# Optimization experiments

Hardware: AMD Instinct MI355X
Metric: run time of the kernel (lower is better)

Reference implementation:

```python
import jax, jax.numpy as jnp
import numpy as np

N, K = 262144, 8
IN_F, H_F, OUT_F = 16, 128, 16
NEG_SLOPE = 0.01  # torch LeakyReLU default


def setup_inputs() -> dict:
    key = jax.random.key(0)
    ks = jax.random.split(key, 10)
    h = jax.random.normal(ks[0], (N, IN_F), dtype=jnp.float32)
    pos = jax.random.uniform(ks[1], (N, 3), dtype=jnp.float32)
    nbr_idx = jax.random.randint(ks[2], (N, K), 0, N)

    def xavier(k, shape):
        fan_in, fan_out = shape[0], shape[1]
        a = jnp.sqrt(6.0 / (fan_in + fan_out))
        return jax.random.uniform(k, shape, jnp.float32, -a, a)

    W0 = xavier(ks[3], (K * IN_F, H_F))
    b0 = xavier(ks[4], (1, H_F))
    W1 = xavier(ks[5], (K * H_F, H_F))
    b1 = xavier(ks[6], (1, H_F))
    W2 = xavier(ks[7], (K * H_F, OUT_F))
    b2 = xavier(ks[8], (1, OUT_F))
    return {"h": h, "pos": pos, "nbr_idx": nbr_idx,
            "W0": W0, "b0": b0, "W1": W1, "b1": b1, "W2": W2, "b2": b2}


def _layer(h, pos, nbr_idx, W, b, activation):
    # gather neighbor messages and positions: [N, K, F], [N, K, 3]
    msgs = h[nbr_idx]
    src_pos = pos[nbr_idx]
    diff = pos[:, None, :] - src_pos                       # [N, K, 3]
    dist = jnp.sqrt(jnp.sum(diff * diff, axis=2, keepdims=True))  # [N, K, 1]
    dist = jnp.where(dist == 0, jnp.float32(0.5), dist)
    wow = (msgs / dist).reshape(h.shape[0], -1)            # [N, K*F]
    out = wow @ W + b
    if activation:
        out = jnp.where(out >= 0, out, NEG_SLOPE * out)
    return out


def reference(h, pos, nbr_idx, W0, b0, W1, b1, W2, b2):
    h1 = _layer(h, pos, nbr_idx, W0, b0, False)   # input layer
    h2 = _layer(h1, pos, nbr_idx, W1, b1, True)   # hidden layer (LeakyReLU)
    h3 = _layer(h2, pos, nbr_idx, W2, b2, False)  # output layer
    return h3
```

## Files before the change

kernel.cpp:

```cpp
#include <hip/hip_runtime.h>
#include <hip/hip_fp16.h>


typedef _Float16 f16x8 __attribute__((ext_vector_type(8)));
typedef float f32x4 __attribute__((ext_vector_type(4)));

#define NNODES 262144

__global__ __launch_bounds__(256) void conv_h_kernel(const float* __restrict__ h,
                                                     __half* __restrict__ h16, int n) {
    int i = blockIdx.x * 256 + threadIdx.x;
    if (i < n) h16[i] = __float2half(h[i]);
}

__global__ __launch_bounds__(256) void prep_edges_kernel(const float* __restrict__ pos,
                                                         const int* __restrict__ nbr,
                                                         __half* __restrict__ invd, int n_edges) {
    int e = blockIdx.x * 256 + threadIdx.x;
    if (e >= n_edges) return;
    int i = e >> 3;
    int n = nbr[e];
    float dx = pos[i * 3 + 0] - pos[n * 3 + 0];
    float dy = pos[i * 3 + 1] - pos[n * 3 + 1];
    float dz = pos[i * 3 + 2] - pos[n * 3 + 2];
    float d = sqrtf(dx * dx + dy * dy + dz * dz);
    if (d == 0.0f) d = 0.5f;
    invd[e] = __float2half((1.0f / d) * 0.00390625f);
}

__global__ __launch_bounds__(256) void shuffle_w_kernel(const float* __restrict__ W,
                                                        __half* __restrict__ Wf,
                                                        int KT, int FO) {
    int e = blockIdx.x * 256 + threadIdx.x;
    if (e >= KT * FO) return;
    int j = e & 7;
    int lane = (e >> 3) & 63;
    int rest = e >> 9;
    int NT = FO >> 4;
    int t = rest % NT;
    int s = rest / NT;
    int k = s * 32 + (lane >> 4) * 8 + j;
    int n = t * 16 + (lane & 15);
    Wf[e] = __float2half(W[k * FO + n]);
}

__global__ __launch_bounds__(256) void layer0_kernel(
    const __half* __restrict__ hprev, const __half* __restrict__ invd,
    const int* __restrict__ nbr, const __half* __restrict__ Wf,
    const float* __restrict__ bias, __half* __restrict__ outp) {
    __shared__ __align__(16) __half Bs[16384];

    const int tid = threadIdx.x;
    const int wave = tid >> 6;
    const int lane = tid & 63;
    const int quad = lane >> 4;
    const int lmod = lane & 15;
    const int mbase = blockIdx.x * 128 + wave * 16 + lmod;

    int idx[2][8];
    f16x8 invr[2];
#pragma unroll
    for (int mt = 0; mt < 2; ++mt) {
        const int m = mbase + mt * 64;
        const int4* nrow = (const int4*)(nbr + (size_t)m * 8);
        const int4 iA = nrow[0];
        const int4 iB = nrow[1];
        idx[mt][0] = iA.x; idx[mt][1] = iA.y; idx[mt][2] = iA.z; idx[mt][3] = iA.w;
        idx[mt][4] = iB.x; idx[mt][5] = iB.y; idx[mt][6] = iB.z; idx[mt][7] = iB.w;
        invr[mt] = *(const f16x8*)(invd + (size_t)m * 8);
    }

    f32x4 acc[2][8];
#pragma unroll
    for (int mt = 0; mt < 2; ++mt)
#pragma unroll
        for (int t = 0; t < 8; ++t) acc[mt][t] = f32x4{0.f, 0.f, 0.f, 0.f};

    {
        const uint4* src = (const uint4*)Wf;
        uint4* dst = (uint4*)Bs;
#pragma unroll
        for (int i = 0; i < 8; ++i) dst[i * 256 + tid] = src[i * 256 + tid];
    }
    __syncthreads();

#pragma unroll
    for (int s = 0; s < 4; ++s) {
        const int nb = 2 * s + (quad >> 1);
        f16x8 as[2];
#pragma unroll
        for (int mt = 0; mt < 2; ++mt) {
            f16x8 av = *(const f16x8*)(hprev + (size_t)idx[mt][nb] * 16 + (quad & 1) * 8);
            as[mt] = av * invr[mt][nb];
        }
#pragma unroll
        for (int t = 0; t < 8; ++t) {
            f16x8 b = *(const f16x8*)(Bs + ((size_t)(s * 8 + t) * 64 + lane) * 8);
#pragma unroll
            for (int mt = 0; mt < 2; ++mt)
                acc[mt][t] = __builtin_amdgcn_mfma_f32_16x16x32_f16(as[mt], b, acc[mt][t], 0, 0, 0);
        }
    }

#pragma unroll
    for (int mt = 0; mt < 2; ++mt) {
        const int rbase = blockIdx.x * 128 + mt * 64 + wave * 16 + quad * 4;
#pragma unroll
        for (int t = 0; t < 8; ++t) {
            const int col = t * 16 + lmod;
            const float bv = bias[col];
#pragma unroll
            for (int rr = 0; rr < 4; ++rr) {
                float v = acc[mt][t][rr] * 256.0f + bv;
                outp[(size_t)(rbase + rr) * 128 + col] = __float2half(v);
            }
        }
    }
}

__device__ __forceinline__ int off16(int seg, int row) {
    return seg * 64 + (row & ~15) + ((row ^ seg) & 15);
}

__global__ __launch_bounds__(256, 3) void layer1_kernel(
    const __half* __restrict__ hprev, const __half* __restrict__ invd,
    const int* __restrict__ nbr, const __half* __restrict__ Wf,
    const float* __restrict__ bias, __half* __restrict__ outp) {
    __shared__ __align__(16) __half As[2][8192];

    const int tid = threadIdx.x;
    const int wave = tid >> 6;
    const int lane = tid & 63;
    const int quad = lane >> 4;
    const int lmod = lane & 15;
    const int rowblk = blockIdx.x * 64;
    const int seg = lmod;

    int srow[4], grow_[4], soff[4];
#pragma unroll
    for (int i = 0; i < 4; ++i) {
        srow[i] = wave * 16 + i * 4 + quad;
        grow_[i] = rowblk + srow[i];
        soff[i] = off16(seg, srow[i]) * 8;
    }

    f16x8 invS[4];
#pragma unroll
    for (int i = 0; i < 4; ++i) invS[i] = *(const f16x8*)(invd + (size_t)grow_[i] * 8);

    int idxA[4], idxB[4], idxR[2][4];
#pragma unroll
    for (int i = 0; i < 4; ++i) {
        idxA[i] = nbr[(size_t)grow_[i] * 8 + 0];
        idxB[i] = nbr[(size_t)grow_[i] * 8 + 1];
        idxR[0][i] = nbr[(size_t)grow_[i] * 8 + 2];
        idxR[1][i] = nbr[(size_t)grow_[i] * 8 + 3];
    }

    const __half* WfB = Wf + ((size_t)(wave * 2) * 64 + lane) * 8;

    f16x8 Bc[4][2], Bn[4][2];
#pragma unroll
    for (int ks = 0; ks < 4; ++ks)
#pragma unroll
        for (int tl = 0; tl < 2; ++tl)
            Bc[ks][tl] = *(const f16x8*)(WfB + (size_t)(ks * 8 + tl) * 512);

    int roff[4][4];
#pragma unroll
    for (int m = 0; m < 4; ++m)
#pragma unroll
        for (int ks = 0; ks < 4; ++ks)
            roff[m][ks] = off16(ks * 4 + quad, m * 16 + lmod) * 8;

    f16x8 ga[2][4];
#pragma unroll
    for (int i = 0; i < 4; ++i)
        ga[0][i] = *(const f16x8*)(hprev + (size_t)idxA[i] * 128 + seg * 8);
#pragma unroll
    for (int i = 0; i < 4; ++i)
        ga[1][i] = *(const f16x8*)(hprev + (size_t)idxB[i] * 128 + seg * 8);

#pragma unroll
    for (int i = 0; i < 4; ++i) {
        f16x8 v = ga[0][i] * invS[i][0];
        *(f16x8*)(&As[0][soff[i]]) = v;
    }
    __syncthreads();

    f32x4 acc[4][2];
#pragma unroll
    for (int m = 0; m < 4; ++m) { acc[m][0] = f32x4{0.f,0.f,0.f,0.f}; acc[m][1] = f32x4{0.f,0.f,0.f,0.f}; }

#pragma unroll
    for (int nb = 0; nb < 8; ++nb) {
        const int cur = nb & 1;
        if (nb < 6) {
#pragma unroll
            for (int i = 0; i < 4; ++i)
                ga[cur][i] = *(const f16x8*)(hprev + (size_t)idxR[cur][i] * 128 + seg * 8);
        }
        if (nb < 4) {
#pragma unroll
            for (int i = 0; i < 4; ++i)
                idxR[cur][i] = nbr[(size_t)grow_[i] * 8 + nb + 4];
        }
        if (nb < 7) {
#pragma unroll
            for (int ks = 0; ks < 4; ++ks)
#pragma unroll
                for (int tl = 0; tl < 2; ++tl)
                    Bn[ks][tl] = *(const f16x8*)(WfB + (size_t)(((nb + 1) * 4 + ks) * 8 + tl) * 512);
        }
#pragma unroll
        for (int m = 0; m < 4; ++m) {
#pragma unroll
            for (int ks = 0; ks < 4; ++ks) {
                f16x8 a = *(const f16x8*)(&As[cur][roff[m][ks]]);
                acc[m][0] = __builtin_amdgcn_mfma_f32_16x16x32_f16(a, Bc[ks][0], acc[m][0], 0, 0, 0);
                acc[m][1] = __builtin_amdgcn_mfma_f32_16x16x32_f16(a, Bc[ks][1], acc[m][1], 0, 0, 0);
            }
        }
        if (nb < 7) {
#pragma unroll
            for (int i = 0; i < 4; ++i) {
                f16x8 v = ga[(nb + 1) & 1][i] * invS[i][nb + 1];
                *(f16x8*)(&As[cur ^ 1][soff[i]]) = v;
            }
#pragma unroll
            for (int ks = 0; ks < 4; ++ks) { Bc[ks][0] = Bn[ks][0]; Bc[ks][1] = Bn[ks][1]; }
            __syncthreads();
        }
    }

#pragma unroll
    for (int m = 0; m < 4; ++m) {
#pragma unroll
        for (int tl = 0; tl < 2; ++tl) {
            const int col = wave * 32 + tl * 16 + lmod;
            const float bv = bias[col];
#pragma unroll
            for (int rr = 0; rr < 4; ++rr) {
                const int grow = rowblk + m * 16 + quad * 4 + rr;
                float v = acc[m][tl][rr] * 256.0f + bv;
                v = (v >= 0.f) ? v : 0.01f * v;
                outp[(size_t)grow * 128 + col] = __float2half(v);
            }
        }
    }
}

__global__ __launch_bounds__(256) void layer2_kernel(
    const __half* __restrict__ hprev, const __half* __restrict__ invd,
    const int* __restrict__ nbr, const __half* __restrict__ Wf,
    const float* __restrict__ bias, float* __restrict__ outp) {
    __shared__ __align__(16) __half Bs[16384];

    const int tid = threadIdx.x;
    const int wave = tid >> 6;
    const int lane = tid & 63;
    const int quad = lane >> 4;
    const int lmod = lane & 15;
    const int m = blockIdx.x * 64 + wave * 16 + lmod;

    const int4* nrow = (const int4*)(nbr + (size_t)m * 8);
    const int4 iA = nrow[0];
    const int4 iB = nrow[1];
    const int idx[8] = {iA.x, iA.y, iA.z, iA.w, iB.x, iB.y, iB.z, iB.w};
    const f16x8 invr = *(const f16x8*)(invd + (size_t)m * 8);

    {
        const uint4* src = (const uint4*)Wf;
        uint4* dst = (uint4*)Bs;
#pragma unroll
        for (int i = 0; i < 8; ++i) dst[i * 256 + tid] = src[i * 256 + tid];
    }
    __syncthreads();

    f16x8 a[4][4];
#pragma unroll
    for (int d = 0; d < 4; ++d)
#pragma unroll
        for (int ks = 0; ks < 4; ++ks)
            a[d][ks] = *(const f16x8*)(hprev + (size_t)idx[d] * 128 + ks * 32 + quad * 8);

    f32x4 acc = f32x4{0.f, 0.f, 0.f, 0.f};
#pragma unroll
    for (int nb = 0; nb < 8; ++nb) {
        const int slot = nb & 3;
#pragma unroll
        for (int ks = 0; ks < 4; ++ks) {
            f16x8 as = a[slot][ks] * invr[nb];
            f16x8 b = *(const f16x8*)(Bs + ((size_t)(nb * 4 + ks) * 64 + lane) * 8);
            acc = __builtin_amdgcn_mfma_f32_16x16x32_f16(as, b, acc, 0, 0, 0);
        }
        if (nb < 4) {
#pragma unroll
            for (int ks = 0; ks < 4; ++ks)
                a[slot][ks] = *(const f16x8*)(hprev + (size_t)idx[nb + 4] * 128 + ks * 32 + quad * 8);
        }
    }

    const int rbase = blockIdx.x * 64 + wave * 16 + quad * 4;
    const float bv = bias[lmod];
#pragma unroll
    for (int rr = 0; rr < 4; ++rr)
        outp[(size_t)(rbase + rr) * 16 + lmod] = acc[rr] * 256.0f + bv;
}

extern "C" void kernel_launch(void* const* d_in, const int* in_sizes, int n_in,
                              void* d_out, int out_size, void* d_ws, size_t ws_size,
                              hipStream_t stream) {
    const float* h   = (const float*)d_in[0];
    const float* pos = (const float*)d_in[1];
    const int*   nbr = (const int*)d_in[2];
    const float* W0  = (const float*)d_in[3];
    const float* b0  = (const float*)d_in[4];
    const float* W1  = (const float*)d_in[5];
    const float* b1  = (const float*)d_in[6];
    const float* W2  = (const float*)d_in[7];
    const float* b2  = (const float*)d_in[8];

    const int N = NNODES;

    char* w = (char*)d_ws;
    __half* h1 = (__half*)w;
    __half* h2 = (__half*)(w + (size_t)67108864);
    __half* invd2 = (__half*)w;
    __half* W2f2  = (__half*)(w + (size_t)4194304);

    char* ob = (char*)d_out;
    __half* invd = (__half*)(ob + 0);
    __half* h16  = (__half*)(ob + 4194304);
    __half* W0f  = (__half*)(ob + 12582912);
    __half* W1f  = (__half*)(ob + 12615680);
    __half* W2f  = (__half*)(ob + 12877824);

    conv_h_kernel<<<(N * 16 + 255) / 256, 256, 0, stream>>>(h, h16, N * 16);
    prep_edges_kernel<<<(N * 8 + 255) / 256, 256, 0, stream>>>(pos, nbr, invd, N * 8);
    shuffle_w_kernel<<<(128 * 128 + 255) / 256, 256, 0, stream>>>(W0, W0f, 128, 128);
    shuffle_w_kernel<<<(1024 * 128 + 255) / 256, 256, 0, stream>>>(W1, W1f, 1024, 128);
    shuffle_w_kernel<<<(1024 * 16 + 255) / 256, 256, 0, stream>>>(W2, W2f, 1024, 16);

    layer0_kernel<<<N / 128, 256, 0, stream>>>(h16, invd, nbr, W0f, b0, h1);
    layer1_kernel<<<N / 64, 256, 0, stream>>>(h1, invd, nbr, W1f, b1, h2);

    (void)hipMemcpyAsync(invd2, invd, 4194304, hipMemcpyDeviceToDevice, stream);
    (void)hipMemcpyAsync(W2f2, W2f, 32768, hipMemcpyDeviceToDevice, stream);

    layer2_kernel<<<N / 64, 256, 0, stream>>>(h2, invd2, nbr, W2f2, b2, (float*)d_out);
}
```

Before: 333.1 us.

## Fuse layer-2 projection into layer1 and replace layer2 with gather-reduce

Layer 2 is reordered. Each node's hidden vector h2 is first projected by the per-slot W2 blocks (128x128 reshaped) inside the layer1 kernel, producing P[node, k*16+c]. A light reduce kernel then gathers the 16-wide slice for each neighbor slot and sums it weighted by the inverse distances. This replaces the heavy gather of 128-wide h2 rows (8 per node) with 16-wide gathers and removes the separate layer2 GEMM. In exchange it adds an extra MFMA stage, an LDS round trip in layer1, and fp16 rounding of the intermediate P.

```diff
diff --git a/kernel.cpp b/kernel.cpp
--- a/kernel.cpp
+++ b/kernel.cpp
@@ -44,6 +44,19 @@
     Wf[e] = __float2half(W[k * FO + n]);
 }
 
+__global__ __launch_bounds__(256) void shuffle_w2s_kernel(const float* __restrict__ W2,
+                                                          __half* __restrict__ Wf) {
+    int e = blockIdx.x * 256 + threadIdx.x;
+    if (e >= 128 * 128) return;
+    int j = e & 7;
+    int lane = (e >> 3) & 63;
+    int rest = e >> 9;
+    int t = rest % 8;
+    int s = rest / 8;
+    int k = s * 32 + (lane >> 4) * 8 + j;
+    Wf[e] = __float2half(W2[(size_t)(t * 128 + k) * 16 + (lane & 15)]);
+}
+
 __global__ __launch_bounds__(256) void layer0_kernel(
     const __half* __restrict__ hprev, const __half* __restrict__ invd,
     const int* __restrict__ nbr, const __half* __restrict__ Wf,
@@ -122,10 +135,11 @@
     return seg * 64 + (row & ~15) + ((row ^ seg) & 15);
 }
 
-__global__ __launch_bounds__(256, 3) void layer1_kernel(
+__global__ __launch_bounds__(256, 3) void layer1p_kernel(
     const __half* __restrict__ hprev, const __half* __restrict__ invd,
     const int* __restrict__ nbr, const __half* __restrict__ Wf,
-    const float* __restrict__ bias, __half* __restrict__ outp) {
+    const __half* __restrict__ Wf2s, const float* __restrict__ bias,
+    __half* __restrict__ Pout) {
     __shared__ __align__(16) __half As[2][8192];
 
     const int tid = threadIdx.x;
@@ -233,79 +247,105 @@
         }
     }
 
+    __half* As0 = &As[0][0];
 #pragma unroll
     for (int m = 0; m < 4; ++m) {
 #pragma unroll
         for (int tl = 0; tl < 2; ++tl) {
             const int col = wave * 32 + tl * 16 + lmod;
             const float bv = bias[col];
+            const int sg = col >> 3;
+            const int jj = col & 7;
+#pragma unroll
+            for (int rr = 0; rr < 4; ++rr) {
+                const int row = m * 16 + quad * 4 + rr;
+                float v = acc[m][tl][rr] * 256.0f + bv;
+                v = (v >= 0.f) ? v : 0.01f * v;
+                As0[off16(sg, row) * 8 + jj] = __float2half(v);
+            }
+        }
+    }
+    __syncthreads();
+
+    const __half* WfB2 = Wf2s + ((size_t)(wave * 2) * 64 + lane) * 8;
+    f16x8 B2[4][2];
+#pragma unroll
+    for (int ks = 0; ks < 4; ++ks)
+#pragma unroll
+        for (int tl = 0; tl < 2; ++tl)
+            B2[ks][tl] = *(const f16x8*)(WfB2 + (size_t)(ks * 8 + tl) * 512);
+
+    f32x4 acc2[4][2];
+#pragma unroll
+    for (int m = 0; m < 4; ++m) { acc2[m][0] = f32x4{0.f,0.f,0.f,0.f}; acc2[m][1] = f32x4{0.f,0.f,0.f,0.f}; }
+#pragma unroll
+    for (int m = 0; m < 4; ++m) {
+#pragma unroll
+        for (int ks = 0; ks < 4; ++ks) {
+            f16x8 a2 = *(const f16x8*)(&As0[roff[m][ks]]);
+            acc2[m][0] = __builtin_amdgcn_mfma_f32_16x16x32_f16(a2, B2[ks][0], acc2[m][0], 0, 0, 0);
+            acc2[m][1] = __builtin_amdgcn_mfma_f32_16x16x32_f16(a2, B2[ks][1], acc2[m][1], 0, 0, 0);
+        }
+    }
+
+#pragma unroll
+    for (int m = 0; m < 4; ++m) {
+#pragma unroll
+        for (int tl = 0; tl < 2; ++tl) {
+            const int col = wave * 32 + tl * 16 + lmod;
 #pragma unroll
             for (int rr = 0; rr < 4; ++rr) {
                 const int grow = rowblk + m * 16 + quad * 4 + rr;
-                float v = acc[m][tl][rr] * 256.0f + bv;
-                v = (v >= 0.f) ? v : 0.01f * v;
-                outp[(size_t)grow * 128 + col] = __float2half(v);
-            }
-        }
-    }
-}
-
-__global__ __launch_bounds__(256) void layer2_kernel(
-    const __half* __restrict__ hprev, const __half* __restrict__ invd,
-    const int* __restrict__ nbr, const __half* __restrict__ Wf,
-    const float* __restrict__ bias, float* __restrict__ outp) {
-    __shared__ __align__(16) __half Bs[16384];
-
-    const int tid = threadIdx.x;
-    const int wave = tid >> 6;
-    const int lane = tid & 63;
-    const int quad = lane >> 4;
-    const int lmod = lane & 15;
-    const int m = blockIdx.x * 64 + wave * 16 + lmod;
-
-    const int4* nrow = (const int4*)(nbr + (size_t)m * 8);
+                Pout[(size_t)grow * 128 + col] = __float2half(acc2[m][tl][rr]);
+            }
+        }
+    }
+}
+
+__global__ __launch_bounds__(256) void reduce_kernel(
+    const __half* __restrict__ P, const __half* __restrict__ invd,
+    const int* __restrict__ nbr, const float* __restrict__ b2,
+    float* __restrict__ outp) {
+    const int d = blockIdx.x * 256 + threadIdx.x;
+
+    const int4* nrow = (const int4*)(nbr + (size_t)d * 8);
     const int4 iA = nrow[0];
     const int4 iB = nrow[1];
     const int idx[8] = {iA.x, iA.y, iA.z, iA.w, iB.x, iB.y, iB.z, iB.w};
-    const f16x8 invr = *(const f16x8*)(invd + (size_t)m * 8);
-
-    {
-        const uint4* src = (const uint4*)Wf;
-        uint4* dst = (uint4*)Bs;
-#pragma unroll
-        for (int i = 0; i < 8; ++i) dst[i * 256 + tid] = src[i * 256 + tid];
-    }
-    __syncthreads();
-
-    f16x8 a[4][4];
-#pragma unroll
-    for (int d = 0; d < 4; ++d)
-#pragma unroll
-        for (int ks = 0; ks < 4; ++ks)
-            a[d][ks] = *(const f16x8*)(hprev + (size_t)idx[d] * 128 + ks * 32 + quad * 8);
-
-    f32x4 acc = f32x4{0.f, 0.f, 0.f, 0.f};
-#pragma unroll
-    for (int nb = 0; nb < 8; ++nb) {
-        const int slot = nb & 3;
-#pragma unroll
-        for (int ks = 0; ks < 4; ++ks) {
-            f16x8 as = a[slot][ks] * invr[nb];
-            f16x8 b = *(const f16x8*)(Bs + ((size_t)(nb * 4 + ks) * 64 + lane) * 8);
-            acc = __builtin_amdgcn_mfma_f32_16x16x32_f16(as, b, acc, 0, 0, 0);
-        }
-        if (nb < 4) {
-#pragma unroll
-            for (int ks = 0; ks < 4; ++ks)
-                a[slot][ks] = *(const f16x8*)(hprev + (size_t)idx[nb + 4] * 128 + ks * 32 + quad * 8);
-        }
-    }
-
-    const int rbase = blockIdx.x * 64 + wave * 16 + quad * 4;
-    const float bv = bias[lmod];
-#pragma unroll
-    for (int rr = 0; rr < 4; ++rr)
-        outp[(size_t)(rbase + rr) * 16 + lmod] = acc[rr] * 256.0f + bv;
+    const f16x8 iv = *(const f16x8*)(invd + (size_t)d * 8);
+
+    f16x8 lo[8], hi[8];
+#pragma unroll
+    for (int k = 0; k < 8; ++k) {
+        const __half* p = P + (size_t)idx[k] * 128 + k * 16;
+        lo[k] = *(const f16x8*)p;
+        hi[k] = *(const f16x8*)(p + 8);
+    }
+
+    float acc[16];
+#pragma unroll
+    for (int c = 0; c < 16; ++c) acc[c] = 0.f;
+#pragma unroll
+    for (int k = 0; k < 8; ++k) {
+        const float w = (float)iv[k];
+#pragma unroll
+        for (int c = 0; c < 8; ++c) {
+            acc[c] += w * (float)lo[k][c];
+            acc[c + 8] += w * (float)hi[k][c];
+        }
+    }
+
+    float4 o[4];
+#pragma unroll
+    for (int q = 0; q < 4; ++q) {
+        o[q].x = acc[q * 4 + 0] * 256.0f + b2[q * 4 + 0];
+        o[q].y = acc[q * 4 + 1] * 256.0f + b2[q * 4 + 1];
+        o[q].z = acc[q * 4 + 2] * 256.0f + b2[q * 4 + 2];
+        o[q].w = acc[q * 4 + 3] * 256.0f + b2[q * 4 + 3];
+    }
+    float4* dst = (float4*)(outp + (size_t)d * 16);
+#pragma unroll
+    for (int q = 0; q < 4; ++q) dst[q] = o[q];
 }
 
 extern "C" void kernel_launch(void* const* d_in, const int* in_sizes, int n_in,
@@ -325,28 +365,26 @@
 
     char* w = (char*)d_ws;
     __half* h1 = (__half*)w;
-    __half* h2 = (__half*)(w + (size_t)67108864);
+    __half* P  = (__half*)(w + (size_t)67108864);
     __half* invd2 = (__half*)w;
-    __half* W2f2  = (__half*)(w + (size_t)4194304);
 
     char* ob = (char*)d_out;
     __half* invd = (__half*)(ob + 0);
     __half* h16  = (__half*)(ob + 4194304);
     __half* W0f  = (__half*)(ob + 12582912);
     __half* W1f  = (__half*)(ob + 12615680);
-    __half* W2f  = (__half*)(ob + 12877824);
+    __half* Wf2s = (__half*)(ob + 12877824);
 
     conv_h_kernel<<<(N * 16 + 255) / 256, 256, 0, stream>>>(h, h16, N * 16);
     prep_edges_kernel<<<(N * 8 + 255) / 256, 256, 0, stream>>>(pos, nbr, invd, N * 8);
     shuffle_w_kernel<<<(128 * 128 + 255) / 256, 256, 0, stream>>>(W0, W0f, 128, 128);
     shuffle_w_kernel<<<(1024 * 128 + 255) / 256, 256, 0, stream>>>(W1, W1f, 1024, 128);
-    shuffle_w_kernel<<<(1024 * 16 + 255) / 256, 256, 0, stream>>>(W2, W2f, 1024, 16);
+    shuffle_w2s_kernel<<<(128 * 128 + 255) / 256, 256, 0, stream>>>(W2, Wf2s);
 
     layer0_kernel<<<N / 128, 256, 0, stream>>>(h16, invd, nbr, W0f, b0, h1);
-    layer1_kernel<<<N / 64, 256, 0, stream>>>(h1, invd, nbr, W1f, b1, h2);
+    layer1p_kernel<<<N / 64, 256, 0, stream>>>(h1, invd, nbr, W1f, Wf2s, b1, P);
 
     (void)hipMemcpyAsync(invd2, invd, 4194304, hipMemcpyDeviceToDevice, stream);
-    (void)hipMemcpyAsync(W2f2, W2f, 32768, hipMemcpyDeviceToDevice, stream);
-
-    layer2_kernel<<<N / 64, 256, 0, stream>>>(h2, invd2, nbr, W2f2, b2, (float*)d_out);
-}
+
+    reduce_kernel<<<N / 256, 256, 0, stream>>>(P, invd2, nbr, b2, (float*)d_out);
+}
```

Measured after the change: 315.1 us. -5.4%, faster.
